# Performance work log

Hardware: AMD Instinct MI355X
Metric: run time of the kernel (lower is better)

Reference implementation:

```python
import jax, jax.numpy as jnp
import numpy as np

N = 50000      # nodes
E = 500000     # edges
D_IN = 64      # node_in_dim
K = 4          # edge_in_dim
H = 64         # node_hidden_dim
C = 40         # num_class
L = 2          # num_layers


def setup_inputs() -> dict:
    key = jax.random.key(0)
    ks = jax.random.split(key, 10)
    node_features = jax.random.normal(ks[0], (N, D_IN), jnp.float32)
    edge_features = jax.random.normal(ks[1], (L, E, K), jnp.float32)
    src = jax.random.randint(ks[2], (E,), 0, N)
    dst = jax.random.randint(ks[3], (E,), 0, N)
    W0 = jax.random.normal(ks[4], (K * D_IN, H), jnp.float32) * 0.05
    b0 = jnp.zeros((H,), jnp.float32)
    W1 = jax.random.normal(ks[5], (K * H, H), jnp.float32) * 0.05
    b1 = jnp.zeros((H,), jnp.float32)
    Wfc = jax.random.normal(ks[6], (H, C), jnp.float32) * 0.05
    bfc = jnp.zeros((C,), jnp.float32)
    return dict(node_features=node_features, edge_features=edge_features,
                src=src, dst=dst, W0=W0, b0=b0, W1=W1, b1=b1, Wfc=Wfc, bfc=bfc)


def reference(node_features, edge_features, src, dst, W0, b0, W1, b1, Wfc, bfc):
    h = node_features  # [N, d]
    ones = jnp.ones((E,), jnp.float32)
    cnt = jnp.maximum(jax.ops.segment_sum(ones, dst, num_segments=N), 1.0)  # in-degree
    for i, (W, b) in enumerate([(W0, b0), (W1, b1)]):
        e = edge_features[i]          # [E, K]
        hs = h[src]                   # [E, d] edge gather of src node features
        d = hs.shape[1]
        # message: relu(Linear(flatten(e[:,:,None] * h[:,None,:])))
        # flatten order is (K, d), so reshape W -> [K, d, H] and contract directly
        Wr = W.reshape(K, d, H)
        m = jax.nn.relu(jnp.einsum('ek,ed,kdh->eh', e, hs, Wr) + b)  # [E, H]
        s = jax.ops.segment_sum(m, dst, num_segments=N)              # scatter-sum
        h = jax.nn.relu(s / cnt[:, None])                            # mailbox mean + relu
    return h @ Wfc + bfc  # [N, C]
```

## Files before the change

### kernel.cpp

```cpp
#include <hip/hip_runtime.h>
#include <hip/hip_fp16.h>

#define N_NODES 50000
#define N_EDGES 500000
#define DIM 64
#define KDIM 4
#define HID 64
#define NCLS 40
#define NBLK ((N_NODES + 255) / 256)
#define NGRP (N_NODES / 16)
#define NUNITS (782 * 2)
#define ZN (50176 + 8 + 256 + 256)

typedef unsigned nuint4 __attribute__((ext_vector_type(4)));

__device__ inline uint4 nt_load4(const uint4* p) {
    nuint4 v = __builtin_nontemporal_load((const nuint4*)p);
    return make_uint4(v.x, v.y, v.z, v.w);
}
__device__ inline void nt_store4(const uint4 v, uint4* p) {
    nuint4 w = { v.x, v.y, v.z, v.w };
    __builtin_nontemporal_store(w, (nuint4*)p);
}

__device__ inline unsigned pack2(float a, float b) {
    __half2 h = __floats2half2_rn(a, b);
    return *(unsigned*)&h;
}
__device__ inline float2 unpack2(unsigned u) {
    __half2 h = *(__half2*)&u;
    return __half22float2(h);
}

__device__ inline void gbar(int* bar, int t) {
    __syncthreads();
    if (t == 0) {
        __threadfence();
        atomicAdd(bar, 1);
        while (__hip_atomic_load(bar, __ATOMIC_RELAXED, __HIP_MEMORY_SCOPE_AGENT)
               < (int)gridDim.x) {
            __builtin_amdgcn_s_sleep(8);
        }
        __threadfence();
    }
    __syncthreads();
}

__device__ inline void transform_unit(const float* __restrict__ hin,
                                      const float* __restrict__ W,
                                      unsigned* __restrict__ y,
                                      int u, int t, __half* sW, float* sh) {
    int nt = u >> 1;
    int kp = u & 1;
    __syncthreads();
    const float4* W4 = (const float4*)(W + (size_t)kp * 8192);
    __half2* sW2 = (__half2*)sW;
#pragma unroll
    for (int i = 0; i < 8; ++i) {
        int idx = t + 256 * i;
        float4 v = W4[idx];
        sW2[2 * idx]     = __floats2half2_rn(v.x, v.y);
        sW2[2 * idx + 1] = __floats2half2_rn(v.z, v.w);
    }
    int n0 = nt * 64;
#pragma unroll
    for (int i = 0; i < 4; ++i) {
        int idx = t + 256 * i;
        int nl = idx >> 4;
        int dg = idx & 15;
        int n = n0 + nl;
        float4 v = make_float4(0.f, 0.f, 0.f, 0.f);
        if (n < N_NODES) v = ((const float4*)hin)[(size_t)n * 16 + dg];
        sh[nl * 65 + dg * 4 + 0] = v.x;
        sh[nl * 65 + dg * 4 + 1] = v.y;
        sh[nl * 65 + dg * 4 + 2] = v.z;
        sh[nl * 65 + dg * 4 + 3] = v.w;
    }
    __syncthreads();

    int nl = t & 31;
    int cg = t >> 5;
    int kl = cg >> 2;
    int hc0 = (cg & 3) * 16;

    float acc0[16], acc1[16];
#pragma unroll
    for (int j = 0; j < 16; ++j) { acc0[j] = 0.f; acc1[j] = 0.f; }

    for (int d = 0; d < 64; ++d) {
        float a0 = sh[nl * 65 + d];
        float a1 = sh[(nl + 32) * 65 + d];
        const __half2* wr = (const __half2*)(sW + kl * 4096 + d * 64 + hc0);
#pragma unroll
        for (int j = 0; j < 8; ++j) {
            float2 w2 = __half22float2(wr[j]);
            acc0[2 * j]     = fmaf(a0, w2.x, acc0[2 * j]);
            acc0[2 * j + 1] = fmaf(a0, w2.y, acc0[2 * j + 1]);
            acc1[2 * j]     = fmaf(a1, w2.x, acc1[2 * j]);
            acc1[2 * j + 1] = fmaf(a1, w2.y, acc1[2 * j + 1]);
        }
    }

    int n_a = n0 + nl, n_b = n0 + nl + 32;
    int cbase = (kp * 2 + kl) * 64 + hc0;
    if (n_a < N_NODES) {
        uint4* o = (uint4*)(y + ((size_t)n_a * 256 + cbase) / 2);
        o[0] = make_uint4(pack2(acc0[0], acc0[1]), pack2(acc0[2], acc0[3]),
                          pack2(acc0[4], acc0[5]), pack2(acc0[6], acc0[7]));
        o[1] = make_uint4(pack2(acc0[8], acc0[9]), pack2(acc0[10], acc0[11]),
                          pack2(acc0[12], acc0[13]), pack2(acc0[14], acc0[15]));
    }
    if (n_b < N_NODES) {
        uint4* o = (uint4*)(y + ((size_t)n_b * 256 + cbase) / 2);
        o[0] = make_uint4(pack2(acc1[0], acc1[1]), pack2(acc1[2], acc1[3]),
                          pack2(acc1[4], acc1[5]), pack2(acc1[6], acc1[7]));
        o[1] = make_uint4(pack2(acc1[8], acc1[9]), pack2(acc1[10], acc1[11]),
                          pack2(acc1[12], acc1[13]), pack2(acc1[14], acc1[15]));
    }
}

__device__ inline void load_edge(const uint4 r, const unsigned* __restrict__ y,
                                 int lane, uint2& q0, uint2& q1, uint2& q2, uint2& q3) {
    int sn = (int)r.x;
    const uint2* yb = (const uint2*)(y + (size_t)sn * 128);
    q0 = yb[lane];
    q1 = yb[16 + lane];
    q2 = yb[32 + lane];
    q3 = yb[48 + lane];
}

__device__ inline void compute_edge(const uint4 r, uint2 q0, uint2 q1, uint2 q2, uint2 q3,
                                    const float4 bias, float4& acc) {
    float2 e01 = unpack2(r.y);
    float2 e23 = unpack2(r.z);
    float2 a0 = unpack2(q0.x), a1 = unpack2(q0.y);
    float2 b0 = unpack2(q1.x), b1 = unpack2(q1.y);
    float2 c0 = unpack2(q2.x), c1 = unpack2(q2.y);
    float2 d0 = unpack2(q3.x), d1 = unpack2(q3.y);

    float4 z = bias;
    z.x = fmaf(e01.x, a0.x, z.x); z.y = fmaf(e01.x, a0.y, z.y);
    z.z = fmaf(e01.x, a1.x, z.z); z.w = fmaf(e01.x, a1.y, z.w);
    z.x = fmaf(e01.y, b0.x, z.x); z.y = fmaf(e01.y, b0.y, z.y);
    z.z = fmaf(e01.y, b1.x, z.z); z.w = fmaf(e01.y, b1.y, z.w);
    z.x = fmaf(e23.x, c0.x, z.x); z.y = fmaf(e23.x, c0.y, z.y);
    z.z = fmaf(e23.x, c1.x, z.z); z.w = fmaf(e23.x, c1.y, z.w);
    z.x = fmaf(e23.y, d0.x, z.x); z.y = fmaf(e23.y, d0.y, z.y);
    z.z = fmaf(e23.y, d1.x, z.z); z.w = fmaf(e23.y, d1.y, z.w);

    acc.x += fmaxf(z.x, 0.f);
    acc.y += fmaxf(z.y, 0.f);
    acc.z += fmaxf(z.z, 0.f);
    acc.w += fmaxf(z.w, 0.f);
}

__device__ inline float4 agg_core(const uint4* __restrict__ rec2,
                                  const int* __restrict__ start,
                                  const int* __restrict__ cnt,
                                  const unsigned* __restrict__ y,
                                  const float* __restrict__ b,
                                  int g, int lane) {
    int s0 = start[g];
    int deg = cnt[g];
    int s1 = s0 + deg;

    float4 bias = ((const float4*)b)[lane];
    float4 acc = make_float4(0.f, 0.f, 0.f, 0.f);

    int i = s0;
    for (; i + 4 <= s1; i += 4) {
        uint4 r0 = nt_load4(&rec2[2 * i + 0]);
        uint4 r1 = nt_load4(&rec2[2 * i + 2]);
        uint4 r2 = nt_load4(&rec2[2 * i + 4]);
        uint4 r3 = nt_load4(&rec2[2 * i + 6]);
        uint2 a0, a1, a2, a3, b0, b1, b2, b3, c0, c1, c2, c3, d0, d1, d2, d3;
        load_edge(r0, y, lane, a0, a1, a2, a3);
        load_edge(r1, y, lane, b0, b1, b2, b3);
        load_edge(r2, y, lane, c0, c1, c2, c3);
        load_edge(r3, y, lane, d0, d1, d2, d3);
        compute_edge(r0, a0, a1, a2, a3, bias, acc);
        compute_edge(r1, b0, b1, b2, b3, bias, acc);
        compute_edge(r2, c0, c1, c2, c3, bias, acc);
        compute_edge(r3, d0, d1, d2, d3, bias, acc);
    }
    if (i + 2 <= s1) {
        uint4 r0 = nt_load4(&rec2[2 * i + 0]);
        uint4 r1 = nt_load4(&rec2[2 * i + 2]);
        uint2 a0, a1, a2, a3, b0, b1, b2, b3;
        load_edge(r0, y, lane, a0, a1, a2, a3);
        load_edge(r1, y, lane, b0, b1, b2, b3);
        compute_edge(r0, a0, a1, a2, a3, bias, acc);
        compute_edge(r1, b0, b1, b2, b3, bias, acc);
        i += 2;
    }
    if (i < s1) {
        uint4 r0 = nt_load4(&rec2[2 * i]);
        uint2 a0, a1, a2, a3;
        load_edge(r0, y, lane, a0, a1, a2, a3);
        compute_edge(r0, a0, a1, a2, a3, bias, acc);
    }

    float inv = 1.0f / (float)(deg > 1 ? deg : 1);
    float4 r;
    r.x = fmaxf(acc.x * inv, 0.f);
    r.y = fmaxf(acc.y * inv, 0.f);
    r.z = fmaxf(acc.z * inv, 0.f);
    r.w = fmaxf(acc.w * inv, 0.f);
    return r;
}

__global__ __launch_bounds__(256, 4) void front_k(const float* __restrict__ nf,
                                                  const float* __restrict__ W0,
                                                  unsigned* __restrict__ y,
                                                  const int* __restrict__ dst,
                                                  int* __restrict__ cnt) {
    __shared__ __align__(16) char smem[33024];
    __half* sW = (__half*)smem;
    float* sh = (float*)(smem + 16384);
    int t = threadIdx.x;

    for (int u = blockIdx.x; u < NUNITS; u += gridDim.x)
        transform_unit(nf, W0, y, u, t, sW, sh);

    int gtid = blockIdx.x * 256 + t;
    int gth = gridDim.x * 256;
    for (int e = gtid; e < N_EDGES; e += gth) atomicAdd(&cnt[dst[e]], 1);
}

__global__ __launch_bounds__(256) void mid_k(const int* __restrict__ cnt,
                                             int* __restrict__ start,
                                             int* __restrict__ cursor,
                                             volatile int* __restrict__ bflag,
                                             volatile int* __restrict__ bval,
                                             int* __restrict__ bar0,
                                             const int* __restrict__ src,
                                             const int* __restrict__ dst,
                                             const float* __restrict__ ef,
                                             uint4* __restrict__ rec) {
    __shared__ int ls[258];
    int b = blockIdx.x, t = threadIdx.x;
    int n = b * 256 + t;
    int v = (n < N_NODES) ? cnt[n] : 0;
    ls[t] = v;
    __syncthreads();
#pragma unroll
    for (int off = 1; off < 256; off <<= 1) {
        int u = (t >= off) ? ls[t - off] : 0;
        __syncthreads();
        ls[t] += u;
        __syncthreads();
    }
    int incl = ls[t];
    int total = ls[255];
    __syncthreads();

    if (t == 0) {
        ((int*)bval)[b] = total;
        __threadfence();
        ((int*)bflag)[b] = 1;
    }

    if (b > 0) {
        for (;;) {
            int f = (t < b) ? bflag[t] : 1;
            if (t == 0) ls[256] = 1;
            __syncthreads();
            if (!f) ls[256] = 0;
            __syncthreads();
            if (ls[256]) break;
        }
        __threadfence();
        int pv = (t < b) ? bval[t] : 0;
        ls[t] = pv;
        __syncthreads();
#pragma unroll
        for (int off = 128; off > 0; off >>= 1) {
            if (t < off) ls[t] += ls[t + off];
            __syncthreads();
        }
        if (t == 0) ls[257] = ls[0];
        __syncthreads();
    } else {
        if (t == 0) ls[257] = 0;
        __syncthreads();
    }

    int excl = ls[257] + incl - v;
    if (n < N_NODES) { start[n] = excl; cursor[n] = excl; }
    if (n == 0) start[N_NODES] = N_EDGES;

    gbar(bar0, t);

    int gtid = b * 256 + t;
    int gth = gridDim.x * 256;
    for (int e = gtid; e < N_EDGES; e += gth) {
        int d = dst[e];
        int pos = atomicAdd(&cursor[d], 1);
        int sn = src[e];
        float4 f0 = ((const float4*)ef)[e];
        float4 f1 = ((const float4*)ef)[N_EDGES + e];
        nt_store4(make_uint4((unsigned)sn, pack2(f0.x, f0.y), pack2(f0.z, f0.w), 0u),
                  &rec[2 * pos]);
        nt_store4(make_uint4((unsigned)sn, pack2(f1.x, f1.y), pack2(f1.z, f1.w), 0u),
                  &rec[2 * pos + 1]);
    }
}

__global__ __launch_bounds__(256) void agg_k(const uint4* __restrict__ rec,
                                             const int* __restrict__ start,
                                             const int* __restrict__ cnt,
                                             const unsigned* __restrict__ y,
                                             const float* __restrict__ b0,
                                             float* __restrict__ hbuf) {
    int t = blockIdx.x * 256 + threadIdx.x;
    int g = t >> 4;
    int lane = t & 15;
    float4 r = agg_core(rec, start, cnt, y, b0, g, lane);
    ((float4*)hbuf)[(size_t)g * 16 + lane] = r;
}

__global__ __launch_bounds__(256, 4) void tr1_k(const float* __restrict__ hbuf,
                                                const float* __restrict__ W1,
                                                unsigned* __restrict__ y) {
    __shared__ __align__(16) char smem[33024];
    __half* sW = (__half*)smem;
    float* sh = (float*)(smem + 16384);
    int t = threadIdx.x;
    for (int u = blockIdx.x; u < NUNITS; u += gridDim.x)
        transform_unit(hbuf, W1, y, u, t, sW, sh);
}

__global__ __launch_bounds__(256) void agg_fc_k(const uint4* __restrict__ rec,
                                                const int* __restrict__ start,
                                                const int* __restrict__ cnt,
                                                const unsigned* __restrict__ y,
                                                const float* __restrict__ b1,
                                                const float* __restrict__ Wfc,
                                                const float* __restrict__ bfc,
                                                float* __restrict__ out) {
    __shared__ float sh_h[16 * 65];
    __shared__ float sWfcT[NCLS * 65];
    __shared__ float sbfc[NCLS];
    int t = threadIdx.x;

    for (int i = t; i < 64 * NCLS; i += 256) {
        int j = i / NCLS;
        int c = i - j * NCLS;
        sWfcT[c * 65 + j] = Wfc[i];
    }
    if (t < NCLS) sbfc[t] = bfc[t];

    int nl = t >> 4;
    int lane = t & 15;
    int g = blockIdx.x * 16 + nl;

    float4 r = agg_core(rec, start, cnt, y, b1, g, lane);
    sh_h[nl * 65 + lane * 4 + 0] = r.x;
    sh_h[nl * 65 + lane * 4 + 1] = r.y;
    sh_h[nl * 65 + lane * 4 + 2] = r.z;
    sh_h[nl * 65 + lane * 4 + 3] = r.w;
    __syncthreads();

    for (int item = t; item < 16 * NCLS; item += 256) {
        int rn = item / NCLS;
        int c = item - rn * NCLS;
        float acc = sbfc[c];
        const float* hr = &sh_h[rn * 65];
        const float* wc = &sWfcT[c * 65];
#pragma unroll
        for (int j = 0; j < 64; ++j) acc = fmaf(hr[j], wc[j], acc);
        __builtin_nontemporal_store(acc, &out[(size_t)(blockIdx.x * 16 + rn) * NCLS + c]);
    }
}

extern "C" void kernel_launch(void* const* d_in, const int* in_sizes, int n_in,
                              void* d_out, int out_size, void* d_ws, size_t ws_size,
                              hipStream_t stream) {
    const float* nf  = (const float*)d_in[0];
    const float* ef  = (const float*)d_in[1];
    const int*   src = (const int*)d_in[2];
    const int*   dst = (const int*)d_in[3];
    const float* W0  = (const float*)d_in[4];
    const float* b0  = (const float*)d_in[5];
    const float* W1  = (const float*)d_in[6];
    const float* b1  = (const float*)d_in[7];
    const float* Wfc = (const float*)d_in[8];
    const float* bfc = (const float*)d_in[9];
    float* out = (float*)d_out;

    char* ws = (char*)d_ws;
    size_t off = 0;
    auto alloc = [&](size_t bytes) -> void* {
        void* p = ws + off;
        off = (off + bytes + 255) & ~(size_t)255;
        return p;
    };
    int*      zbuf   = (int*)     alloc((size_t)ZN * 4);
    int*      cnt    = zbuf;
    int*      bar    = zbuf + 50176;
    int*      bflag  = zbuf + 50176 + 8;
    int*      bval   = zbuf + 50176 + 8 + 256;
    int*      start  = (int*)     alloc((size_t)(N_NODES + 1) * 4);
    int*      cursor = (int*)     alloc((size_t)N_NODES * 4);
    uint4*    rec    = (uint4*)   alloc((size_t)N_EDGES * 32);
    unsigned* y      = (unsigned*)alloc((size_t)N_NODES * 256 * 2);
    float*    hbuf   = (float*)   alloc((size_t)N_NODES * 64 * 4);

    (void)hipMemsetAsync(zbuf, 0, (size_t)ZN * 4, stream);

    front_k<<<1024, 256, 0, stream>>>(nf, W0, y, dst, cnt);
    mid_k<<<NBLK, 256, 0, stream>>>(cnt, start, cursor, bflag, bval, bar + 0,
                                    src, dst, ef, rec);
    agg_k<<<NGRP, 256, 0, stream>>>(rec, start, cnt, y, b0, hbuf);
    tr1_k<<<NUNITS, 256, 0, stream>>>(hbuf, W1, y);
    agg_fc_k<<<NGRP, 256, 0, stream>>>(rec + 1, start, cnt, y, b1, Wfc, bfc, out);
}
```

Baseline: 326.2 us.

## Split fused scan/scatter kernel into separate launches instead of grid barrier

```diff
diff --git a/kernel.cpp b/kernel.cpp
--- a/kernel.cpp
+++ b/kernel.cpp
@@ -10,7 +10,6 @@
 #define NBLK ((N_NODES + 255) / 256)
 #define NGRP (N_NODES / 16)
 #define NUNITS (782 * 2)
-#define ZN (50176 + 8 + 256 + 256)
 
 typedef unsigned nuint4 __attribute__((ext_vector_type(4)));
 
@@ -30,20 +29,6 @@
 __device__ inline float2 unpack2(unsigned u) {
     __half2 h = *(__half2*)&u;
     return __half22float2(h);
-}
-
-__device__ inline void gbar(int* bar, int t) {
-    __syncthreads();
-    if (t == 0) {
-        __threadfence();
-        atomicAdd(bar, 1);
-        while (__hip_atomic_load(bar, __ATOMIC_RELAXED, __HIP_MEMORY_SCOPE_AGENT)
-               < (int)gridDim.x) {
-            __builtin_amdgcn_s_sleep(8);
-        }
-        __threadfence();
-    }
-    __syncthreads();
 }
 
 __device__ inline void transform_unit(const float* __restrict__ hin,
@@ -227,19 +212,12 @@
     for (int e = gtid; e < N_EDGES; e += gth) atomicAdd(&cnt[dst[e]], 1);
 }
 
-__global__ __launch_bounds__(256) void mid_k(const int* __restrict__ cnt,
-                                             int* __restrict__ start,
-                                             int* __restrict__ cursor,
-                                             volatile int* __restrict__ bflag,
-                                             volatile int* __restrict__ bval,
-                                             int* __restrict__ bar0,
-                                             const int* __restrict__ src,
-                                             const int* __restrict__ dst,
-                                             const float* __restrict__ ef,
-                                             uint4* __restrict__ rec) {
-    __shared__ int ls[258];
-    int b = blockIdx.x, t = threadIdx.x;
-    int n = b * 256 + t;
+__global__ __launch_bounds__(256) void blk_scan_k(const int* __restrict__ cnt,
+                                                  int* __restrict__ esc,
+                                                  int* __restrict__ bsum) {
+    __shared__ int ls[256];
+    int t = threadIdx.x;
+    int n = blockIdx.x * 256 + t;
     int v = (n < N_NODES) ? cnt[n] : 0;
     ls[t] = v;
     __syncthreads();
@@ -250,50 +228,44 @@
         ls[t] += u;
         __syncthreads();
     }
-    int incl = ls[t];
-    int total = ls[255];
-    __syncthreads();
-
-    if (t == 0) {
-        ((int*)bval)[b] = total;
-        __threadfence();
-        ((int*)bflag)[b] = 1;
-    }
-
-    if (b > 0) {
-        for (;;) {
-            int f = (t < b) ? bflag[t] : 1;
-            if (t == 0) ls[256] = 1;
-            __syncthreads();
-            if (!f) ls[256] = 0;
-            __syncthreads();
-            if (ls[256]) break;
-        }
-        __threadfence();
-        int pv = (t < b) ? bval[t] : 0;
-        ls[t] = pv;
+    if (n < N_NODES) esc[n] = ls[t] - v;
+    if (t == 255) bsum[blockIdx.x] = ls[255];
+}
+
+__global__ __launch_bounds__(256) void bsum_scan_k(const int* __restrict__ bsum,
+                                                   int* __restrict__ boff,
+                                                   int* __restrict__ start) {
+    __shared__ int ls[256];
+    int t = threadIdx.x;
+    int v = (t < NBLK) ? bsum[t] : 0;
+    ls[t] = v;
+    __syncthreads();
+#pragma unroll
+    for (int off = 1; off < 256; off <<= 1) {
+        int u = (t >= off) ? ls[t - off] : 0;
         __syncthreads();
-#pragma unroll
-        for (int off = 128; off > 0; off >>= 1) {
-            if (t < off) ls[t] += ls[t + off];
-            __syncthreads();
-        }
-        if (t == 0) ls[257] = ls[0];
+        ls[t] += u;
         __syncthreads();
-    } else {
-        if (t == 0) ls[257] = 0;
-        __syncthreads();
-    }
-
-    int excl = ls[257] + incl - v;
-    if (n < N_NODES) { start[n] = excl; cursor[n] = excl; }
-    if (n == 0) start[N_NODES] = N_EDGES;
-
-    gbar(bar0, t);
-
-    int gtid = b * 256 + t;
-    int gth = gridDim.x * 256;
-    for (int e = gtid; e < N_EDGES; e += gth) {
+    }
+    if (t < NBLK) boff[t] = ls[t] - v;
+    if (t == 0) start[N_NODES] = N_EDGES;
+}
+
+__global__ void finalize_k(const int* __restrict__ esc, const int* __restrict__ boff,
+                           int* __restrict__ start, int* __restrict__ cursor) {
+    int n = blockIdx.x * 256 + threadIdx.x;
+    if (n < N_NODES) {
+        int s = esc[n] + boff[blockIdx.x];
+        start[n] = s;
+        cursor[n] = s;
+    }
+}
+
+__global__ void scatter_k(const int* __restrict__ src, const int* __restrict__ dst,
+                          const float* __restrict__ ef, int* __restrict__ cursor,
+                          uint4* __restrict__ rec) {
+    int e = blockIdx.x * 256 + threadIdx.x;
+    if (e < N_EDGES) {
         int d = dst[e];
         int pos = atomicAdd(&cursor[d], 1);
         int sn = src[e];
@@ -395,22 +367,23 @@
         off = (off + bytes + 255) & ~(size_t)255;
         return p;
     };
-    int*      zbuf   = (int*)     alloc((size_t)ZN * 4);
-    int*      cnt    = zbuf;
-    int*      bar    = zbuf + 50176;
-    int*      bflag  = zbuf + 50176 + 8;
-    int*      bval   = zbuf + 50176 + 8 + 256;
+    int*      cnt    = (int*)     alloc((size_t)N_NODES * 4);
+    int*      esc    = (int*)     alloc((size_t)N_NODES * 4);
+    int*      bsum   = (int*)     alloc((size_t)NBLK * 4);
+    int*      boff   = (int*)     alloc((size_t)NBLK * 4);
     int*      start  = (int*)     alloc((size_t)(N_NODES + 1) * 4);
     int*      cursor = (int*)     alloc((size_t)N_NODES * 4);
     uint4*    rec    = (uint4*)   alloc((size_t)N_EDGES * 32);
     unsigned* y      = (unsigned*)alloc((size_t)N_NODES * 256 * 2);
     float*    hbuf   = (float*)   alloc((size_t)N_NODES * 64 * 4);
 
-    (void)hipMemsetAsync(zbuf, 0, (size_t)ZN * 4, stream);
+    (void)hipMemsetAsync(cnt, 0, (size_t)N_NODES * 4, stream);
 
     front_k<<<1024, 256, 0, stream>>>(nf, W0, y, dst, cnt);
-    mid_k<<<NBLK, 256, 0, stream>>>(cnt, start, cursor, bflag, bval, bar + 0,
-                                    src, dst, ef, rec);
+    blk_scan_k<<<NBLK, 256, 0, stream>>>(cnt, esc, bsum);
+    bsum_scan_k<<<1, 256, 0, stream>>>(bsum, boff, start);
+    finalize_k<<<NBLK, 256, 0, stream>>>(esc, boff, start, cursor);
+    scatter_k<<<(N_EDGES + 255) / 256, 256, 0, stream>>>(src, dst, ef, cursor, rec);
     agg_k<<<NGRP, 256, 0, stream>>>(rec, start, cnt, y, b0, hbuf);
     tr1_k<<<NUNITS, 256, 0, stream>>>(hbuf, W1, y);
     agg_fc_k<<<NGRP, 256, 0, stream>>>(rec + 1, start, cnt, y, b1, Wfc, bfc, out);
```

New measurement: 302.1 us. 1.08x faster.
